# Kernel tuning notes

Measured on AMD Instinct MI355X. Metric: run time of the kernel, lower is better.

The kernel has to match this reference:

```python
import jax, jax.numpy as jnp
from jax import lax
import numpy as np

DIM = 384
H = W = 32
B = 32
HALF = DIM // 2


def _parc(x, pe, w, b, axis):
    """Global circular depthwise conv along `axis` (2=H, 3=W). w: (C,1,kh,kw)."""
    x = x + pe
    k = x.shape[axis]
    if axis == 2:
        x_cat = jnp.concatenate([x, x[:, :, : k - 1, :]], axis=2)
    else:
        x_cat = jnp.concatenate([x, x[:, :, :, : k - 1]], axis=3)
    out = lax.conv_general_dilated(
        x_cat, w, window_strides=(1, 1), padding='VALID',
        dimension_numbers=('NCHW', 'OIHW', 'NCHW'),
        feature_group_count=x.shape[1])
    return out + b[None, :, None, None]


def setup_inputs() -> dict:
    key = jax.random.key(0)
    ks = jax.random.split(key, 12)
    std = 0.02
    return {
        'x': jax.random.normal(ks[0], (B, DIM, H, W), jnp.float32),
        'pe_h': std * jax.random.normal(ks[1], (1, HALF, H, 1), jnp.float32),
        'w_h': std * jax.random.normal(ks[2], (HALF, 1, H, 1), jnp.float32),
        'b_h': jnp.zeros((HALF,), jnp.float32),
        'pe_w': std * jax.random.normal(ks[3], (1, HALF, 1, W), jnp.float32),
        'w_w': std * jax.random.normal(ks[4], (HALF, 1, 1, W), jnp.float32),
        'b_w': jnp.zeros((HALF,), jnp.float32),
        'ln_w': jnp.ones((DIM,), jnp.float32),
        'ln_b': jnp.zeros((DIM,), jnp.float32),
        'w1': std * jax.random.normal(ks[5], (DIM, 4 * DIM), jnp.float32),
        'b1': jnp.zeros((4 * DIM,), jnp.float32),
        'w2': std * jax.random.normal(ks[6], (4 * DIM, DIM), jnp.float32),
        'b2': jnp.zeros((DIM,), jnp.float32),
        'gamma': 1e-6 * jnp.ones((DIM,), jnp.float32),
    }


def reference(x, pe_h, w_h, b_h, pe_w, w_w, b_w, ln_w, ln_b, w1, b1, w2, b2, gamma):
    inp = x
    half = x.shape[1] // 2
    x_h = _parc(x[:, :half], pe_h, w_h, b_h, axis=2)
    x_w = _parc(x[:, half:], pe_w, w_w, b_w, axis=3)
    y = jnp.concatenate([x_h, x_w], axis=1).transpose(0, 2, 3, 1)  # NHWC
    # LayerNorm over channels (eps=1e-6)
    mu = y.mean(-1, keepdims=True)
    var = ((y - mu) ** 2).mean(-1, keepdims=True)
    y = (y - mu) / jnp.sqrt(var + 1e-6) * ln_w + ln_b
    # inverted MLP: dim -> 4*dim -> dim with exact GELU
    y = jax.nn.gelu(jnp.dot(y, w1) + b1, approximate=False)
    y = jnp.dot(y, w2) + b2
    y = gamma * y
    return inp + y.transpose(0, 3, 1, 2)
```

## Files before the change

### kernel.cpp

```cpp
#include <hip/hip_runtime.h>


typedef __attribute__((ext_vector_type(8))) short short8;
typedef __attribute__((ext_vector_type(4))) float f32x4;
typedef __attribute__((ext_vector_type(4))) int int4v;

__device__ __forceinline__ float bf2f(unsigned short u) {
  union { unsigned int i; float f; } v; v.i = ((unsigned int)u) << 16; return v.f;
}
__device__ __forceinline__ unsigned short f2bf(float f) {
  union { float f; unsigned int i; } v; v.f = f;
  unsigned int r = v.i + 0x7FFFu + ((v.i >> 16) & 1u);
  return (unsigned short)(r >> 16);
}
__device__ __forceinline__ long lo64(int4v v) {
  return (long)(((unsigned long)(unsigned)v[1] << 32) | (unsigned)v[0]);
}
__device__ __forceinline__ long hi64(int4v v) {
  return (long)(((unsigned long)(unsigned)v[3] << 32) | (unsigned)v[2]);
}

#if defined(__has_builtin)
#if __has_builtin(__builtin_amdgcn_global_load_lds)
#define HAS_GLL 1
#endif
#endif
#ifndef HAS_GLL
#define HAS_GLL 0
#endif

#if HAS_GLL
__device__ __forceinline__ void gload16(const void* g, void* l) {
  __builtin_amdgcn_global_load_lds((const __attribute__((address_space(1))) void*)g,
                                   (__attribute__((address_space(3))) void*)l, 16, 0, 0);
}
#else
__device__ __forceinline__ void gload16(const void* g, void* l) {
  *(f32x4*)l = *(const f32x4*)g;
}
#endif

template <int N>
__device__ __forceinline__ void wait_vm() {
  asm volatile("s_waitcnt vmcnt(%0)" :: "n"(N) : "memory");
}
__device__ __forceinline__ void barrier_raw() {
  __builtin_amdgcn_s_barrier();
  __builtin_amdgcn_sched_barrier(0);
}

__device__ __forceinline__ float fast_gelu(float h) {
  const float e = __builtin_amdgcn_exp2f(-2.4554005f * h);
  return h * __builtin_amdgcn_rcpf(1.f + e);
}

__device__ __forceinline__ int pk4(float a, float b, float c, float d) {
  int r = __builtin_amdgcn_cvt_pk_fp8_f32(a, b, 0, false);
  return __builtin_amdgcn_cvt_pk_fp8_f32(c, d, r, true);
}

__global__ __launch_bounds__(256) void pack_kernel(
    const float* __restrict__ w1, const float* __restrict__ w2,
    char* __restrict__ w1p, char* __restrict__ w2p) {
  const int t = threadIdx.x;
  const int bid = blockIdx.x;
  float v[64];
  if (bid < 36) {
    const int kt = bid % 6, hg = bid / 6;
    const int h = hg * 256 + t;
    #pragma unroll
    for (int k = 0; k < 64; ++k) v[k] = w1[(size_t)(kt * 64 + k) * 1536 + h];
    const int swz = (h >> 1) & 3;
    char* rowp = w1p + ((size_t)(kt * 1536 + h)) * 64;
    #pragma unroll
    for (int k0 = 0; k0 < 64; k0 += 4) {
      const int chunk = ((k0 >> 3) & 3) ^ swz;
      const int sub = (k0 & 7) + (k0 >= 32 ? 8 : 0);
      *(int*)(rowp + chunk * 16 + sub) = pk4(v[k0], v[k0 + 1], v[k0 + 2], v[k0 + 3]);
    }
  } else {
    const int kt = bid - 36;
    for (int c = t; c < 384; c += 256) {
      #pragma unroll
      for (int k = 0; k < 64; ++k) v[k] = w2[(size_t)(kt * 64 + k) * 384 + c];
      const int swz = (c >> 1) & 3;
      char* rowp = w2p + ((size_t)(kt * 384 + c)) * 64;
      #pragma unroll
      for (int k0 = 0; k0 < 64; k0 += 4) {
        const int chunk = ((k0 >> 3) & 3) ^ swz;
        const int sub = (k0 & 7) + (k0 >= 32 ? 8 : 0);
        *(int*)(rowp + chunk * 16 + sub) = pk4(v[k0], v[k0 + 1], v[k0 + 2], v[k0 + 3]);
      }
    }
  }
}

__global__ __launch_bounds__(256) void conv_kernel(
    const float* __restrict__ x,
    const float* __restrict__ pe_h, const float* __restrict__ w_h, const float* __restrict__ b_h,
    const float* __restrict__ pe_w, const float* __restrict__ w_w, const float* __restrict__ b_w,
    unsigned short* __restrict__ convout) {
  __shared__ float wt_s[8][32], pe_s[8][32], pc_s[8][32];
  const int t = threadIdx.x;
  const int bid = blockIdx.x;
  const int b = bid / 48, g = bid % 48;
  const int c0 = g << 3;
  const bool ish = (c0 < 192);
  const int cl = t >> 5, q = t & 31;
  {
    const int c = c0 + cl;
    if (ish) { wt_s[cl][q] = w_h[(c << 5) + q];           pe_s[cl][q] = pe_h[(c << 5) + q]; }
    else     { const int cc = c - 192;
               wt_s[cl][q] = w_w[(cc << 5) + q];          pe_s[cl][q] = pe_w[(cc << 5) + q]; }
  }
  __syncthreads();
  {
    float s = ish ? b_h[c0 + cl] : b_w[c0 + cl - 192];
    #pragma unroll
    for (int i = 0; i < 32; ++i) s += pe_s[cl][(q + i) & 31] * wt_s[cl][i];
    pc_s[cl][q] = s;
  }
  __syncthreads();
  const float* xp = x + ((size_t)(b * 384 + c0 + cl) << 10);
  float col[32];
  if (ish) {
    #pragma unroll
    for (int j = 0; j < 32; ++j) col[j] = xp[(j << 5) + q];
  } else {
    const float* rp = xp + (q << 5);
    #pragma unroll
    for (int j4 = 0; j4 < 8; ++j4) {
      f32x4 v = *(const f32x4*)&rp[j4 << 2];
      col[j4 * 4 + 0] = v[0]; col[j4 * 4 + 1] = v[1];
      col[j4 * 4 + 2] = v[2]; col[j4 * 4 + 3] = v[3];
    }
  }
  float wr[32];
  #pragma unroll
  for (int i = 0; i < 32; ++i) wr[i] = wt_s[cl][i];
  float o[32];
  #pragma unroll
  for (int oo = 0; oo < 32; ++oo) o[oo] = pc_s[cl][oo];
  #pragma unroll
  for (int i = 0; i < 32; ++i)
    #pragma unroll
    for (int oo = 0; oo < 32; ++oo)
      o[oo] = fmaf(col[(oo + i) & 31], wr[i], o[oo]);
  unsigned short* op = convout + ((size_t)(b * 384 + c0 + cl) << 10);
  if (ish) {
    #pragma unroll
    for (int oo = 0; oo < 32; ++oo) op[(oo << 5) + q] = f2bf(o[oo]);
  } else {
    #pragma unroll
    for (int j8 = 0; j8 < 4; ++j8) {
      short8 p;
      #pragma unroll
      for (int j = 0; j < 8; ++j) p[j] = (short)f2bf(o[j8 * 8 + j]);
      *(short8*)&op[(q << 5) + j8 * 8] = p;
    }
  }
}

__global__ __launch_bounds__(256) void ln_stats_kernel(
    const unsigned short* __restrict__ conv,
    float* __restrict__ mu, float* __restrict__ rs) {
  __shared__ float sums[4][64], sqs[4][64];
  const int tid = threadIdx.x;
  const int lane = tid & 63;
  const int w = tid >> 6;
  const int px = blockIdx.x * 64 + lane;
  const int b = px >> 10, hw = px & 1023;
  const unsigned short* cp = conv + (((size_t)(b * 384 + w * 96)) << 10) + hw;
  float s = 0.f, ss = 0.f;
  #pragma unroll 8
  for (int k = 0; k < 96; ++k) {
    float v = bf2f(cp[(size_t)k << 10]);
    s += v; ss = fmaf(v, v, ss);
  }
  sums[w][lane] = s; sqs[w][lane] = ss;
  __syncthreads();
  if (tid < 64) {
    const float st = sums[0][tid] + sums[1][tid] + sums[2][tid] + sums[3][tid];
    const float sst = sqs[0][tid] + sqs[1][tid] + sqs[2][tid] + sqs[3][tid];
    const float m = st * (1.f / 384.f);
    const float var = sst * (1.f / 384.f) - m * m;
    mu[blockIdx.x * 64 + tid] = m;
    rs[blockIdx.x * 64 + tid] = rsqrtf(var + 1e-6f);
  }
}

__global__ __launch_bounds__(256) void ln_pack_kernel(
    const unsigned short* __restrict__ conv,
    const float* __restrict__ mu, const float* __restrict__ rs,
    char* __restrict__ ylnp,
    const float* __restrict__ ln_w, const float* __restrict__ ln_b) {
  __shared__ float lw[64], lb[64];
  const int kt = blockIdx.y;
  const int t = threadIdx.x;
  if (t < 64) { lw[t] = ln_w[kt * 64 + t]; lb[t] = ln_b[kt * 64 + t]; }
  __syncthreads();
  const int px = blockIdx.x * 256 + t;
  const int b = px >> 10, hw = px & 1023;
  const unsigned short* cp = conv + (((size_t)(b * 384 + kt * 64)) << 10) + hw;
  const float m = mu[px], r = rs[px];
  float ov[64];
  #pragma unroll
  for (int k = 0; k < 64; ++k) {
    const float v = bf2f(cp[(size_t)k << 10]);
    ov[k] = (v - m) * r * lw[k] + lb[k];
  }
  const int swz = (px >> 1) & 3;
  char* rowp = ylnp + ((size_t)(kt * 32768 + px)) * 64;
  #pragma unroll
  for (int q = 0; q < 4; ++q) {
    int4v d;
    d[0] = pk4(ov[q * 8 + 0], ov[q * 8 + 1], ov[q * 8 + 2], ov[q * 8 + 3]);
    d[1] = pk4(ov[q * 8 + 4], ov[q * 8 + 5], ov[q * 8 + 6], ov[q * 8 + 7]);
    d[2] = pk4(ov[32 + q * 8 + 0], ov[32 + q * 8 + 1], ov[32 + q * 8 + 2], ov[32 + q * 8 + 3]);
    d[3] = pk4(ov[32 + q * 8 + 4], ov[32 + q * 8 + 5], ov[32 + q * 8 + 6], ov[32 + q * 8 + 7]);
    *(int4v*)(rowp + ((q ^ swz) << 4)) = d;
  }
}

template <int EPI, int KDIM, int AROWS>
__global__ __launch_bounds__(256, 3) void gemm_kernel(
    const char* __restrict__ Ab, const char* __restrict__ Bb,
    char* __restrict__ Hout8, const float* __restrict__ bias,
    const float* __restrict__ gamma, const float* __restrict__ xres,
    float* __restrict__ out, int px0, int btot, int boff, int nwg, int nx) {
  extern __shared__ char lds[];
  constexpr int BM = 128, BN = 128;
  constexpr int NB = 3, DEPTH = 2;
  constexpr int NT = KDIM / 64;
  constexpr int SLOT = (BM + BN) * 64;
  constexpr int CH = (BM + BN) * 4 / 256;
  const int tid = threadIdx.x;
  const int lane = tid & 63;
  const int wid = tid >> 6;
  const int wm = wid >> 1, wn = wid & 1;
  const int fr = lane & 15;
  const int kq = lane >> 4;
  const int bid = blockIdx.x;
  const int q = nwg >> 3, r = nwg & 7;
  const int xcd = bid & 7, idx = bid >> 3;
  const int lg = (xcd < r ? xcd * (q + 1) : r * (q + 1) + (xcd - r) * q) + idx;
  const int xb = lg % nx, yb = lg / nx;
  const int arow0 = xb * BM;
  const int brow0 = yb * BN;

  f32x4 acc[4][4] = {};

  auto stage = [&](int tile) {
    char* sl = lds + (size_t)(tile % NB) * SLOT;
    #pragma unroll
    for (int i = 0; i < 2; ++i) {
      const int c = i * 256 + tid;
      const int row = c >> 2, ch = c & 3;
      gload16(Ab + ((size_t)(tile * AROWS + arow0 + row)) * 64 + (ch << 4),
              sl + c * 16);
    }
    #pragma unroll
    for (int i = 0; i < 2; ++i) {
      const int c = i * 256 + tid;
      const int row = c >> 2, ch = c & 3;
      gload16(Bb + ((size_t)(tile * (size_t)btot + boff + brow0 + row)) * 64 + (ch << 4),
              sl + (BM * 4 + c) * 16);
    }
  };

  auto step = [&](int t, int stage_tile) {
    const char* slp = lds + (size_t)(t % NB) * SLOT;
    int4v a1[4], b1v[4];
    #pragma unroll
    for (int m = 0; m < 4; ++m) {
      const int rr = wm * 64 + m * 16 + fr;
      a1[m] = *(const int4v*)(slp + rr * 64 + ((kq ^ ((rr >> 1) & 3)) << 4));
    }
    #pragma unroll
    for (int n = 0; n < 4; ++n) {
      const int rr = wn * 64 + n * 16 + fr;
      b1v[n] = *(const int4v*)(slp + BM * 64 + rr * 64 + ((kq ^ ((rr >> 1) & 3)) << 4));
    }
    if (stage_tile >= 0) stage(stage_tile);
    __builtin_amdgcn_s_setprio(1);
    #pragma unroll
    for (int m = 0; m < 4; ++m)
      #pragma unroll
      for (int n = 0; n < 4; ++n) {
        acc[m][n] = __builtin_amdgcn_mfma_f32_16x16x32_fp8_fp8(
            lo64(a1[m]), lo64(b1v[n]), acc[m][n], 0, 0, 0);
        acc[m][n] = __builtin_amdgcn_mfma_f32_16x16x32_fp8_fp8(
            hi64(a1[m]), hi64(b1v[n]), acc[m][n], 0, 0, 0);
      }
    __builtin_amdgcn_s_setprio(0);
  };

  #pragma unroll
  for (int d = 0; d < DEPTH; ++d) stage(d);
  wait_vm<CH * (DEPTH - 1)>();
  barrier_raw();

  #pragma unroll 1
  for (int t = 0; t < NT - DEPTH; ++t) {
    step(t, t + DEPTH);
    wait_vm<CH * (DEPTH - 1)>();
    barrier_raw();
  }
  step(NT - 2, -1);
  wait_vm<0>();
  barrier_raw();
  step(NT - 1, -1);

  if (EPI == 0) {
    const int htile = (arow0 + wm * 64) >> 6;
    #pragma unroll
    for (int m = 0; m < 4; ++m) {
      const int hb = arow0 + wm * 64 + m * 16 + kq * 4;
      const float bv0 = bias[hb + 0], bv1 = bias[hb + 1];
      const float bv2 = bias[hb + 2], bv3 = bias[hb + 3];
      const int chunk_base = (2 * m + (kq >> 1)) & 3;
      const int sub = (m >= 2 ? 8 : 0) + (kq & 1) * 4;
      #pragma unroll
      for (int n = 0; n < 4; ++n) {
        const int px = brow0 + wn * 64 + n * 16 + fr;
        const int d = pk4(fast_gelu(acc[m][n][0] + bv0), fast_gelu(acc[m][n][1] + bv1),
                          fast_gelu(acc[m][n][2] + bv2), fast_gelu(acc[m][n][3] + bv3));
        const int chunk = chunk_base ^ ((px >> 1) & 3);
        *(int*)(Hout8 + ((size_t)(htile * btot + px)) * 64 + chunk * 16 + sub) = d;
      }
    }
  } else {
    #pragma unroll
    for (int m = 0; m < 4; ++m) {
      #pragma unroll
      for (int rr = 0; rr < 4; ++rr) {
        const int c = arow0 + wm * 64 + m * 16 + kq * 4 + rr;
        const float gv = gamma[c];
        const float bv = bias[c];
        #pragma unroll
        for (int n = 0; n < 4; ++n) {
          const int px = px0 + brow0 + wn * 64 + n * 16 + fr;
          const int bb = px >> 10, hw = px & 1023;
          const size_t oi = (((size_t)(bb * 384 + c)) << 10) + hw;
          out[oi] = xres[oi] + gv * (acc[m][n][rr] + bv);
        }
      }
    }
  }
}

extern "C" void kernel_launch(void* const* d_in, const int* in_sizes, int n_in,
                              void* d_out, int out_size, void* d_ws, size_t ws_size,
                              hipStream_t stream) {
  (void)in_sizes; (void)n_in; (void)out_size;
  const float* x     = (const float*)d_in[0];
  const float* pe_h  = (const float*)d_in[1];
  const float* w_h   = (const float*)d_in[2];
  const float* b_h   = (const float*)d_in[3];
  const float* pe_w  = (const float*)d_in[4];
  const float* w_w   = (const float*)d_in[5];
  const float* b_w   = (const float*)d_in[6];
  const float* ln_w  = (const float*)d_in[7];
  const float* ln_b  = (const float*)d_in[8];
  const float* w1    = (const float*)d_in[9];
  const float* b1    = (const float*)d_in[10];
  const float* w2    = (const float*)d_in[11];
  const float* b2    = (const float*)d_in[12];
  const float* gamma = (const float*)d_in[13];
  float* out = (float*)d_out;
  char* ws = (char*)d_ws;

  char*           W1P  = ws;
  char*           W2P  = ws + 589824;
  float*          MU   = (float*)(ws + 1179648);
  float*          RS   = (float*)(ws + 1310720);
  char*           YLNP = ws + 1441792;
  unsigned short* CONV = (unsigned short*)(ws + 14024704);
  char*           HID  = ws + 14024704;

  int G = 32;
  while (G > 2) {
    size_t hid = (size_t)G * 1572864ull;
    size_t need = 14024704ull + (hid > 25165824ull ? hid : 25165824ull);
    if (need <= ws_size) break;
    G -= 2;
  }

  constexpr int LDS = (128 + 128) * 64 * 3;

  pack_kernel<<<dim3(60), dim3(256), 0, stream>>>(w1, w2, W1P, W2P);
  conv_kernel<<<dim3(1536), dim3(256), 0, stream>>>(x, pe_h, w_h, b_h, pe_w, w_w, b_w, CONV);
  ln_stats_kernel<<<dim3(512), dim3(256), 0, stream>>>(CONV, MU, RS);
  ln_pack_kernel<<<dim3(128, 6), dim3(256), 0, stream>>>(CONV, MU, RS, YLNP, ln_w, ln_b);
  for (int i0 = 0; i0 < 32; i0 += G) {
    const int gi = (32 - i0 < G) ? (32 - i0) : G;
    const int Mpx = gi * 1024;
    {
      const int nwg = 12 * (Mpx / 128);
      gemm_kernel<0, 384, 1536><<<dim3(nwg), dim3(256), LDS, stream>>>(
          W1P, YLNP, HID, b1, nullptr, nullptr, nullptr,
          0, Mpx, i0 * 1024, nwg, 12);
    }
    {
      const int nwg = 3 * (Mpx / 128);
      gemm_kernel<1, 1536, 384><<<dim3(nwg), dim3(256), LDS, stream>>>(
          W2P, HID, nullptr, b2, gamma, x, out, i0 * 1024, Mpx, 0, nwg, 3);
    }
  }
}
```

Baseline: 113.2 us.

## Switch FP8 GEMMs to 32x32x64 scaled MFMA with matching operand layout

Replaces the pairs of 16x16x32 FP8 MFMAs with the gfx950 scaled 32x32x64 f8f6f4 MFMA, using unit scales. The packing of weights, LN outputs and the hidden activations is reordered so each lane's 32 contiguous K bytes match the new operand layout, and the epilogues are rewritten for the 32x32 accumulator layout. Fewer, larger MFMAs and fewer LDS reads per K step should cut issue overhead. The hidden-buffer stride is now passed separately, and the main loop is unrolled by three.

```diff
diff --git a/kernel.cpp b/kernel.cpp
--- a/kernel.cpp
+++ b/kernel.cpp
@@ -3,7 +3,9 @@
 
 typedef __attribute__((ext_vector_type(8))) short short8;
 typedef __attribute__((ext_vector_type(4))) float f32x4;
+typedef __attribute__((ext_vector_type(16))) float f32x16;
 typedef __attribute__((ext_vector_type(4))) int int4v;
+typedef __attribute__((ext_vector_type(8))) int i32x8;
 
 __device__ __forceinline__ float bf2f(unsigned short u) {
   union { unsigned int i; float f; } v; v.i = ((unsigned int)u) << 16; return v.f;
@@ -12,12 +14,6 @@
   union { float f; unsigned int i; } v; v.f = f;
   unsigned int r = v.i + 0x7FFFu + ((v.i >> 16) & 1u);
   return (unsigned short)(r >> 16);
-}
-__device__ __forceinline__ long lo64(int4v v) {
-  return (long)(((unsigned long)(unsigned)v[1] << 32) | (unsigned)v[0]);
-}
-__device__ __forceinline__ long hi64(int4v v) {
-  return (long)(((unsigned long)(unsigned)v[3] << 32) | (unsigned)v[2]);
 }
 
 #if defined(__has_builtin)
@@ -58,6 +54,8 @@
   int r = __builtin_amdgcn_cvt_pk_fp8_f32(a, b, 0, false);
   return __builtin_amdgcn_cvt_pk_fp8_f32(c, d, r, true);
 }
+
+#define SCL1 0x7F7F7F7F
 
 __global__ __launch_bounds__(256) void pack_kernel(
     const float* __restrict__ w1, const float* __restrict__ w2,
@@ -74,9 +72,8 @@
     char* rowp = w1p + ((size_t)(kt * 1536 + h)) * 64;
     #pragma unroll
     for (int k0 = 0; k0 < 64; k0 += 4) {
-      const int chunk = ((k0 >> 3) & 3) ^ swz;
-      const int sub = (k0 & 7) + (k0 >= 32 ? 8 : 0);
-      *(int*)(rowp + chunk * 16 + sub) = pk4(v[k0], v[k0 + 1], v[k0 + 2], v[k0 + 3]);
+      const int chunk = (k0 >> 4) ^ swz;
+      *(int*)(rowp + chunk * 16 + (k0 & 12)) = pk4(v[k0], v[k0 + 1], v[k0 + 2], v[k0 + 3]);
     }
   } else {
     const int kt = bid - 36;
@@ -87,9 +84,8 @@
       char* rowp = w2p + ((size_t)(kt * 384 + c)) * 64;
       #pragma unroll
       for (int k0 = 0; k0 < 64; k0 += 4) {
-        const int chunk = ((k0 >> 3) & 3) ^ swz;
-        const int sub = (k0 & 7) + (k0 >= 32 ? 8 : 0);
-        *(int*)(rowp + chunk * 16 + sub) = pk4(v[k0], v[k0 + 1], v[k0 + 2], v[k0 + 3]);
+        const int chunk = (k0 >> 4) ^ swz;
+        *(int*)(rowp + chunk * 16 + (k0 & 12)) = pk4(v[k0], v[k0 + 1], v[k0 + 2], v[k0 + 3]);
       }
     }
   }
@@ -214,10 +210,10 @@
   #pragma unroll
   for (int q = 0; q < 4; ++q) {
     int4v d;
-    d[0] = pk4(ov[q * 8 + 0], ov[q * 8 + 1], ov[q * 8 + 2], ov[q * 8 + 3]);
-    d[1] = pk4(ov[q * 8 + 4], ov[q * 8 + 5], ov[q * 8 + 6], ov[q * 8 + 7]);
-    d[2] = pk4(ov[32 + q * 8 + 0], ov[32 + q * 8 + 1], ov[32 + q * 8 + 2], ov[32 + q * 8 + 3]);
-    d[3] = pk4(ov[32 + q * 8 + 4], ov[32 + q * 8 + 5], ov[32 + q * 8 + 6], ov[32 + q * 8 + 7]);
+    d[0] = pk4(ov[q * 16 + 0],  ov[q * 16 + 1],  ov[q * 16 + 2],  ov[q * 16 + 3]);
+    d[1] = pk4(ov[q * 16 + 4],  ov[q * 16 + 5],  ov[q * 16 + 6],  ov[q * 16 + 7]);
+    d[2] = pk4(ov[q * 16 + 8],  ov[q * 16 + 9],  ov[q * 16 + 10], ov[q * 16 + 11]);
+    d[3] = pk4(ov[q * 16 + 12], ov[q * 16 + 13], ov[q * 16 + 14], ov[q * 16 + 15]);
     *(int4v*)(rowp + ((q ^ swz) << 4)) = d;
   }
 }
@@ -227,19 +223,20 @@
     const char* __restrict__ Ab, const char* __restrict__ Bb,
     char* __restrict__ Hout8, const float* __restrict__ bias,
     const float* __restrict__ gamma, const float* __restrict__ xres,
-    float* __restrict__ out, int px0, int btot, int boff, int nwg, int nx) {
+    float* __restrict__ out, int px0, int bstride, int boff, int hstride,
+    int nwg, int nx) {
   extern __shared__ char lds[];
   constexpr int BM = 128, BN = 128;
   constexpr int NB = 3, DEPTH = 2;
   constexpr int NT = KDIM / 64;
   constexpr int SLOT = (BM + BN) * 64;
-  constexpr int CH = (BM + BN) * 4 / 256;
+  constexpr int CH = 4;
   const int tid = threadIdx.x;
   const int lane = tid & 63;
   const int wid = tid >> 6;
   const int wm = wid >> 1, wn = wid & 1;
-  const int fr = lane & 15;
-  const int kq = lane >> 4;
+  const int lane31 = lane & 31;
+  const int kh = lane >> 5;
   const int bid = blockIdx.x;
   const int q = nwg >> 3, r = nwg & 7;
   const int xcd = bid & 7, idx = bid >> 3;
@@ -248,7 +245,23 @@
   const int arow0 = xb * BM;
   const int brow0 = yb * BN;
 
-  f32x4 acc[4][4] = {};
+  f32x16 acc[2][2] = {};
+
+  int aoff[2][2], boffl[2][2];
+  #pragma unroll
+  for (int m = 0; m < 2; ++m) {
+    const int row = wm * 64 + m * 32 + lane31;
+    const int s = (row >> 1) & 3;
+    aoff[m][0] = row * 64 + (((2 * kh + 0) ^ s) << 4);
+    aoff[m][1] = row * 64 + (((2 * kh + 1) ^ s) << 4);
+  }
+  #pragma unroll
+  for (int n = 0; n < 2; ++n) {
+    const int row = wn * 64 + n * 32 + lane31;
+    const int s = (row >> 1) & 3;
+    boffl[n][0] = BM * 64 + row * 64 + (((2 * kh + 0) ^ s) << 4);
+    boffl[n][1] = BM * 64 + row * 64 + (((2 * kh + 1) ^ s) << 4);
+  }
 
   auto stage = [&](int tile) {
     char* sl = lds + (size_t)(tile % NB) * SLOT;
@@ -263,35 +276,36 @@
     for (int i = 0; i < 2; ++i) {
       const int c = i * 256 + tid;
       const int row = c >> 2, ch = c & 3;
-      gload16(Bb + ((size_t)(tile * (size_t)btot + boff + brow0 + row)) * 64 + (ch << 4),
+      gload16(Bb + ((size_t)tile * bstride + boff + brow0 + row) * 64 + (ch << 4),
               sl + (BM * 4 + c) * 16);
     }
   };
 
   auto step = [&](int t, int stage_tile) {
     const char* slp = lds + (size_t)(t % NB) * SLOT;
-    int4v a1[4], b1v[4];
-    #pragma unroll
-    for (int m = 0; m < 4; ++m) {
-      const int rr = wm * 64 + m * 16 + fr;
-      a1[m] = *(const int4v*)(slp + rr * 64 + ((kq ^ ((rr >> 1) & 3)) << 4));
-    }
-    #pragma unroll
-    for (int n = 0; n < 4; ++n) {
-      const int rr = wn * 64 + n * 16 + fr;
-      b1v[n] = *(const int4v*)(slp + BM * 64 + rr * 64 + ((kq ^ ((rr >> 1) & 3)) << 4));
+    i32x8 av[2], bv[2];
+    #pragma unroll
+    for (int m = 0; m < 2; ++m) {
+      int4v p0 = *(const int4v*)(slp + aoff[m][0]);
+      int4v p1 = *(const int4v*)(slp + aoff[m][1]);
+      av[m][0] = p0[0]; av[m][1] = p0[1]; av[m][2] = p0[2]; av[m][3] = p0[3];
+      av[m][4] = p1[0]; av[m][5] = p1[1]; av[m][6] = p1[2]; av[m][7] = p1[3];
+    }
+    #pragma unroll
+    for (int n = 0; n < 2; ++n) {
+      int4v p0 = *(const int4v*)(slp + boffl[n][0]);
+      int4v p1 = *(const int4v*)(slp + boffl[n][1]);
+      bv[n][0] = p0[0]; bv[n][1] = p0[1]; bv[n][2] = p0[2]; bv[n][3] = p0[3];
+      bv[n][4] = p1[0]; bv[n][5] = p1[1]; bv[n][6] = p1[2]; bv[n][7] = p1[3];
     }
     if (stage_tile >= 0) stage(stage_tile);
     __builtin_amdgcn_s_setprio(1);
     #pragma unroll
-    for (int m = 0; m < 4; ++m)
-      #pragma unroll
-      for (int n = 0; n < 4; ++n) {
-        acc[m][n] = __builtin_amdgcn_mfma_f32_16x16x32_fp8_fp8(
-            lo64(a1[m]), lo64(b1v[n]), acc[m][n], 0, 0, 0);
-        acc[m][n] = __builtin_amdgcn_mfma_f32_16x16x32_fp8_fp8(
-            hi64(a1[m]), hi64(b1v[n]), acc[m][n], 0, 0, 0);
-      }
+    for (int m = 0; m < 2; ++m)
+      #pragma unroll
+      for (int n = 0; n < 2; ++n)
+        acc[m][n] = __builtin_amdgcn_mfma_scale_f32_32x32x64_f8f6f4(
+            av[m], bv[n], acc[m][n], 0, 0, 0, SCL1, 0, SCL1);
     __builtin_amdgcn_s_setprio(0);
   };
 
@@ -300,7 +314,7 @@
   wait_vm<CH * (DEPTH - 1)>();
   barrier_raw();
 
-  #pragma unroll 1
+  #pragma unroll 3
   for (int t = 0; t < NT - DEPTH; ++t) {
     step(t, t + DEPTH);
     wait_vm<CH * (DEPTH - 1)>();
@@ -312,37 +326,45 @@
   step(NT - 1, -1);
 
   if (EPI == 0) {
-    const int htile = (arow0 + wm * 64) >> 6;
-    #pragma unroll
-    for (int m = 0; m < 4; ++m) {
-      const int hb = arow0 + wm * 64 + m * 16 + kq * 4;
-      const float bv0 = bias[hb + 0], bv1 = bias[hb + 1];
-      const float bv2 = bias[hb + 2], bv3 = bias[hb + 3];
-      const int chunk_base = (2 * m + (kq >> 1)) & 3;
-      const int sub = (m >= 2 ? 8 : 0) + (kq & 1) * 4;
-      #pragma unroll
-      for (int n = 0; n < 4; ++n) {
-        const int px = brow0 + wn * 64 + n * 16 + fr;
-        const int d = pk4(fast_gelu(acc[m][n][0] + bv0), fast_gelu(acc[m][n][1] + bv1),
-                          fast_gelu(acc[m][n][2] + bv2), fast_gelu(acc[m][n][3] + bv3));
-        const int chunk = chunk_base ^ ((px >> 1) & 3);
-        *(int*)(Hout8 + ((size_t)(htile * btot + px)) * 64 + chunk * 16 + sub) = d;
+    const int kt = (arow0 + wm * 64) >> 6;
+    #pragma unroll
+    for (int m = 0; m < 2; ++m) {
+      #pragma unroll
+      for (int G = 0; G < 4; ++G) {
+        const int bytepos = m * 32 + 8 * G + 4 * kh;
+        const int hg = arow0 + wm * 64 + bytepos;
+        const float b0 = bias[hg + 0], b1v = bias[hg + 1];
+        const float b2v = bias[hg + 2], b3v = bias[hg + 3];
+        const int chunk = bytepos >> 4, sub = bytepos & 15;
+        #pragma unroll
+        for (int n = 0; n < 2; ++n) {
+          const int px = brow0 + wn * 64 + n * 32 + lane31;
+          const int d = pk4(fast_gelu(acc[m][n][4 * G + 0] + b0),
+                            fast_gelu(acc[m][n][4 * G + 1] + b1v),
+                            fast_gelu(acc[m][n][4 * G + 2] + b2v),
+                            fast_gelu(acc[m][n][4 * G + 3] + b3v));
+          const int pchunk = chunk ^ ((px >> 1) & 3);
+          *(int*)(Hout8 + ((size_t)(kt * hstride + px)) * 64 + pchunk * 16 + sub) = d;
+        }
       }
     }
   } else {
     #pragma unroll
-    for (int m = 0; m < 4; ++m) {
-      #pragma unroll
-      for (int rr = 0; rr < 4; ++rr) {
-        const int c = arow0 + wm * 64 + m * 16 + kq * 4 + rr;
-        const float gv = gamma[c];
-        const float bv = bias[c];
+    for (int m = 0; m < 2; ++m) {
+      #pragma unroll
+      for (int G = 0; G < 4; ++G) {
         #pragma unroll
-        for (int n = 0; n < 4; ++n) {
-          const int px = px0 + brow0 + wn * 64 + n * 16 + fr;
-          const int bb = px >> 10, hw = px & 1023;
-          const size_t oi = (((size_t)(bb * 384 + c)) << 10) + hw;
-          out[oi] = xres[oi] + gv * (acc[m][n][rr] + bv);
+        for (int j = 0; j < 4; ++j) {
+          const int c = arow0 + wm * 64 + m * 32 + 8 * G + 4 * kh + j;
+          const float gv = gamma[c];
+          const float bv = bias[c];
+          #pragma unroll
+          for (int n = 0; n < 2; ++n) {
+            const int px = px0 + brow0 + wn * 64 + n * 32 + lane31;
+            const int bb = px >> 10, hw = px & 1023;
+            const size_t oi = (((size_t)(bb * 384 + c)) << 10) + hw;
+            out[oi] = xres[oi] + gv * (acc[m][n][4 * G + j] + bv);
+          }
         }
       }
     }
@@ -399,12 +421,12 @@
       const int nwg = 12 * (Mpx / 128);
       gemm_kernel<0, 384, 1536><<<dim3(nwg), dim3(256), LDS, stream>>>(
           W1P, YLNP, HID, b1, nullptr, nullptr, nullptr,
-          0, Mpx, i0 * 1024, nwg, 12);
+          0, 32768, i0 * 1024, Mpx, nwg, 12);
     }
     {
       const int nwg = 3 * (Mpx / 128);
       gemm_kernel<1, 1536, 384><<<dim3(nwg), dim3(256), LDS, stream>>>(
-          W2P, HID, nullptr, b2, gamma, x, out, i0 * 1024, Mpx, 0, nwg, 3);
-    }
-  }
-}
+          W2P, HID, nullptr, b2, gamma, x, out, i0 * 1024, Mpx, 0, 0, nwg, 3);
+    }
+  }
+}
```

New measurement: 116.7 us. +3.1%, slower.
